# Optimization experiments

Hardware: AMD Instinct MI355X
Metric: run time of the kernel (lower is better)

The kernel has to match this reference:

```python
import jax, jax.numpy as jnp
import numpy as np

B, T, LQ, LC = 8, 256, 20, 10
DIM, H = 128, 8
VDIM, WDIM, CDIM = 1024, 300, 50
WORDS, CHARS = 10000, 100


def _build_edges(T, B):
    """Replicates build_graph_edges(hops=2) + build_semantic_edges + build_query_edges,
    then expand_edge_index_for_batch with num_nodes = T + 1.  Static numpy (jit-safe)."""
    N = T + 1
    es = []
    for h in (1, 2):  # temporal edges, 2 hops (indices replicate original code exactly)
        i = np.arange(T - h)
        es += [np.stack([i, i + h]), np.stack([i + h, i])]
    i = np.arange(T)  # query<->segment edges inside build_graph_edges
    z = np.zeros(T, dtype=np.int64)
    es += [np.stack([z, i + 1]), np.stack([i + 1, z])]
    temporal = np.concatenate(es, axis=1)
    a, b = np.triu_indices(T, k=1)  # torch.combinations(arange(T), r=2)
    sem = np.concatenate([np.stack([a, b]), np.stack([b, a])], axis=1)
    qe = np.stack([np.concatenate([[0], np.arange(1, T + 1)]),
                   np.concatenate([np.arange(1, T + 1), [0]])])
    off = (np.arange(B, dtype=np.int64) * N)[None, :, None]
    expand = lambda e: (e[:, None, :].astype(np.int64) + off).reshape(2, -1)
    return np.concatenate([expand(temporal), expand(sem), expand(qe)], axis=1)


def setup_inputs() -> dict:
    key = jax.random.key(0)
    ks = jax.random.split(key, 16)
    w = lambda k, shape: jax.random.normal(k, shape, jnp.float32) * 0.02
    return {
        "word_ids": jax.random.randint(ks[0], (B, LQ), 0, WORDS),
        "char_ids": jax.random.randint(ks[1], (B, LQ, LC), 0, CHARS),
        "video_features": jax.random.normal(ks[2], (B, T, VDIM), jnp.float32),
        "v_mask": jnp.ones((B, T), jnp.float32),
        "q_mask": jnp.ones((B, LQ), jnp.float32),
        "word_emb": w(ks[3], (WORDS, WDIM)),
        "char_emb": w(ks[4], (CHARS, CDIM)),
        "W_embed": w(ks[5], (WDIM + CDIM, DIM)), "b_embed": jnp.zeros((DIM,), jnp.float32),
        "W_vproj": w(ks[6], (VDIM, DIM)), "b_vproj": jnp.zeros((DIM,), jnp.float32),
        "W_enc": w(ks[7], (DIM, DIM)), "b_enc": jnp.zeros((DIM,), jnp.float32),
        "Wq": w(ks[8], (DIM, DIM)), "bq": jnp.zeros((DIM,), jnp.float32),
        "Wk": w(ks[9], (DIM, DIM)), "bk": jnp.zeros((DIM,), jnp.float32),
        "Wv": w(ks[10], (DIM, DIM)), "bv": jnp.zeros((DIM,), jnp.float32),
        "Wskip": w(ks[11], (DIM, DIM)), "bskip": jnp.zeros((DIM,), jnp.float32),
        "W_start": w(ks[12], (DIM, 1)), "b_start": jnp.zeros((1,), jnp.float32),
        "W_end": w(ks[13], (DIM, 1)), "b_end": jnp.zeros((1,), jnp.float32),
    }


def reference(word_ids, char_ids, video_features, v_mask, q_mask,
              word_emb, char_emb, W_embed, b_embed, W_vproj, b_vproj,
              W_enc, b_enc, Wq, bq, Wk, bk, Wv, bv, Wskip, bskip,
              W_start, b_start, W_end, b_end):
    enc = lambda x, m: jax.nn.relu(x @ W_enc + b_enc) * m[..., None]  # shared feature encoder (stand-in)
    # video branch
    vfeat = enc(video_features @ W_vproj + b_vproj, v_mask)            # [B, T, DIM]
    # query branch: word + char embeddings -> dim, encode, mean-pool
    qemb = jnp.concatenate([word_emb[word_ids], char_emb[char_ids].mean(axis=2)], axis=-1)
    qfeat = enc(qemb @ W_embed + b_embed, q_mask).mean(axis=1)         # [B, DIM]
    nodes = jnp.concatenate([qfeat[:, None, :], vfeat], axis=1)        # [B, N, DIM], N = T+1
    Bn, N, _ = nodes.shape
    Nn = Bn * N
    xf = nodes.reshape(Nn, DIM)
    edges = jnp.asarray(_build_edges(N - 1, Bn))                       # [2, E] static
    src, dst = edges[0], edges[1]                                      # PyG: messages x_j=src -> target i=dst
    hd = DIM // H
    q = (xf @ Wq + bq).reshape(Nn, H, hd)
    k = (xf @ Wk + bk).reshape(Nn, H, hd)
    v = (xf @ Wv + bv).reshape(Nn, H, hd)
    # TransformerConv: per-edge attention logits, segment-softmax over incoming edges
    logits = (q[dst] * k[src]).sum(-1) / float(np.sqrt(hd))            # [E, H]
    mx = jax.ops.segment_max(logits, dst, num_segments=Nn)
    ex = jnp.exp(logits - mx[dst])
    den = jax.ops.segment_sum(ex, dst, num_segments=Nn)
    alpha = ex / (den[dst] + 1e-16)
    agg = jax.ops.segment_sum(alpha[:, :, None] * v[src], dst, num_segments=Nn)  # [Nn, H, hd]
    out = agg.reshape(Nn, DIM) + xf @ Wskip + bskip                    # root_weight skip connection
    out = out.reshape(Bn, N, DIM)
    start_logits = (out[:, 1:] @ W_start + b_start)[..., 0]            # [B, T]
    end_logits = (out[:, 1:] @ W_end + b_end)[..., 0]                  # [B, T]
    return start_logits, end_logits
```

## Files before the change

kernel.cpp:

```cpp
#include <hip/hip_runtime.h>
#include <hip/hip_bf16.h>
#include <math.h>

#define B_ 8
#define T_ 256
#define LQ_ 20
#define LC_ 10
#define DIM_ 128
#define N_ 257
#define NN_ (B_*N_)

#define FMA4(a, s, ww) { (a).x += (s)*(ww).x; (a).y += (s)*(ww).y; (a).z += (s)*(ww).z; (a).w += (s)*(ww).w; }

__global__ __launch_bounds__(512) void kNODE(
    const float* __restrict__ video, const float* __restrict__ Wv,
    const float* __restrict__ bvp,
    const float* __restrict__ We, const float* __restrict__ be,
    const float* __restrict__ vmask,
    const int* __restrict__ word_ids, const int* __restrict__ char_ids,
    const float* __restrict__ word_emb, const float* __restrict__ char_emb,
    const float* __restrict__ W_embed, const float* __restrict__ b_embed,
    const float* __restrict__ q_mask,
    const float* __restrict__ Wq, const float* __restrict__ bq,
    const float* __restrict__ Wk, const float* __restrict__ bk,
    const float* __restrict__ Wvv, const float* __restrict__ bval,
    const float* __restrict__ Ws, const float* __restrict__ bs,
    float* __restrict__ q, float* __restrict__ k,
    float* __restrict__ v, float* __restrict__ sk,
    float* __restrict__ eq)
{
  __shared__ __align__(16) float smem_f[19008];
  float4* ps4 = reinterpret_cast<float4*>(smem_f);
  float* hl = smem_f + 16896;
  float* xe = smem_f + 17952;
  const int blk = blockIdx.x, tid = threadIdx.x;
  const float* Wm[4] = {Wq, Wk, Wvv, Ws};
  const float* bm[4] = {bq, bk, bval, bs};
  float* om[4] = {q, k, v, sk};

  if (blk < 256) {
    const int r0 = blk * 8;
    {
      const float4* src = reinterpret_cast<const float4*>(video + (size_t)r0 * 1024);
      #pragma unroll
      for (int i = 0; i < 4; ++i) {
        const int idx4 = tid + i * 512;
        const int r = idx4 >> 8, f = idx4 & 255;
        *reinterpret_cast<float4*>(&smem_f[r * 1028 + f * 4]) = src[r * 256 + f];
      }
    }
    __syncthreads();
    const int c4 = tid & 31, ks = tid >> 5;
    float4 acc[8];
    #pragma unroll
    for (int r = 0; r < 8; ++r) acc[r] = float4{0.f, 0.f, 0.f, 0.f};
    {
      const float4* W4 = reinterpret_cast<const float4*>(Wv) + c4;
      for (int kc = 0; kc < 16; ++kc) {
        const int k0 = ks * 64 + kc * 4;
        const float4 w0 = W4[(size_t)(k0 + 0) * 32];
        const float4 w1 = W4[(size_t)(k0 + 1) * 32];
        const float4 w2 = W4[(size_t)(k0 + 2) * 32];
        const float4 w3 = W4[(size_t)(k0 + 3) * 32];
        #pragma unroll
        for (int r = 0; r < 8; ++r) {
          const float4 rv = *reinterpret_cast<const float4*>(&smem_f[r * 1028 + k0]);
          FMA4(acc[r], rv.x, w0); FMA4(acc[r], rv.y, w1);
          FMA4(acc[r], rv.z, w2); FMA4(acc[r], rv.w, w3);
        }
      }
    }
    __syncthreads();
    #pragma unroll
    for (int r = 0; r < 8; ++r) ps4[(ks * 8 + r) * 33 + c4] = acc[r];
    __syncthreads();
    if (tid < 256) {
      const int r = tid >> 5, c = tid & 31;
      float4 s = reinterpret_cast<const float4*>(bvp)[c];
      #pragma unroll
      for (int ke = 0; ke < 16; ++ke) {
        const float4 p = ps4[(ke * 8 + r) * 33 + c];
        s.x += p.x; s.y += p.y; s.z += p.z; s.w += p.w;
      }
      *reinterpret_cast<float4*>(&hl[r * 132 + c * 4]) = s;
    }
    __syncthreads();
    #pragma unroll
    for (int r = 0; r < 8; ++r) acc[r] = float4{0.f, 0.f, 0.f, 0.f};
    {
      const float4* We4 = reinterpret_cast<const float4*>(We) + c4;
      #pragma unroll
      for (int kc = 0; kc < 2; ++kc) {
        const int k0 = ks * 8 + kc * 4;
        const float4 w0 = We4[(size_t)(k0 + 0) * 32];
        const float4 w1 = We4[(size_t)(k0 + 1) * 32];
        const float4 w2 = We4[(size_t)(k0 + 2) * 32];
        const float4 w3 = We4[(size_t)(k0 + 3) * 32];
        #pragma unroll
        for (int r = 0; r < 8; ++r) {
          const float4 rv = *reinterpret_cast<const float4*>(&hl[r * 132 + k0]);
          FMA4(acc[r], rv.x, w0); FMA4(acc[r], rv.y, w1);
          FMA4(acc[r], rv.z, w2); FMA4(acc[r], rv.w, w3);
        }
      }
    }
    #pragma unroll
    for (int r = 0; r < 8; ++r) ps4[(ks * 8 + r) * 33 + c4] = acc[r];
    __syncthreads();
    if (tid < 256) {
      const int r = tid >> 5, c = tid & 31;
      float4 s = reinterpret_cast<const float4*>(be)[c];
      #pragma unroll
      for (int ke = 0; ke < 16; ++ke) {
        const float4 p = ps4[(ke * 8 + r) * 33 + c];
        s.x += p.x; s.y += p.y; s.z += p.z; s.w += p.w;
      }
      const float mk = vmask[r0 + r];
      s.x = fmaxf(s.x, 0.f) * mk; s.y = fmaxf(s.y, 0.f) * mk;
      s.z = fmaxf(s.z, 0.f) * mk; s.w = fmaxf(s.w, 0.f) * mk;
      *reinterpret_cast<float4*>(&xe[r * 132 + c * 4]) = s;
    }
    __syncthreads();
    const int m = ks >> 2, keP = ks & 3;
    #pragma unroll
    for (int r = 0; r < 8; ++r) acc[r] = float4{0.f, 0.f, 0.f, 0.f};
    {
      const float4* Wp4 = reinterpret_cast<const float4*>(Wm[m]) + c4;
      #pragma unroll
      for (int kc = 0; kc < 8; ++kc) {
        const int k0 = keP * 32 + kc * 4;
        const float4 w0 = Wp4[(size_t)(k0 + 0) * 32];
        const float4 w1 = Wp4[(size_t)(k0 + 1) * 32];
        const float4 w2 = Wp4[(size_t)(k0 + 2) * 32];
        const float4 w3 = Wp4[(size_t)(k0 + 3) * 32];
        #pragma unroll
        for (int r = 0; r < 8; ++r) {
          const float4 rv = *reinterpret_cast<const float4*>(&xe[r * 132 + k0]);
          FMA4(acc[r], rv.x, w0); FMA4(acc[r], rv.y, w1);
          FMA4(acc[r], rv.z, w2); FMA4(acc[r], rv.w, w3);
        }
      }
    }
    #pragma unroll
    for (int r = 0; r < 8; ++r) ps4[(ks * 8 + r) * 33 + c4] = acc[r];
    __syncthreads();
    #pragma unroll
    for (int it = 0; it < 2; ++it) {
      const int id = tid + it * 512;
      const int mm = id >> 8, r = (id >> 5) & 7, c = id & 31;
      float4 s = reinterpret_cast<const float4*>(bm[mm])[c];
      #pragma unroll
      for (int ke = 0; ke < 4; ++ke) {
        const float4 p = ps4[((mm * 4 + ke) * 8 + r) * 33 + c];
        s.x += p.x; s.y += p.y; s.z += p.z; s.w += p.w;
      }
      const int vr = r0 + r;
      const int node = (vr >> 8) * 257 + 1 + (vr & 255);
      *reinterpret_cast<float4*>(om[mm] + (size_t)node * 128 + 4 * c) = s;
    }
  } else {
    const int qi = blk - 256;
    const int b = qi / 20, lq = qi - b * 20;
    float* emb = smem_f;
    float* ps  = emb + 352;
    float* hq  = emb + 608;
    float* pe  = emb + 736;
    const int wid = word_ids[b * LQ_ + lq];
    for (int m2 = tid; m2 < 300; m2 += 512) emb[m2] = word_emb[(size_t)wid * 300 + m2];
    if (tid < 50) {
      float s = 0.f;
      #pragma unroll
      for (int l = 0; l < 10; ++l) {
        const int cid = char_ids[(b * LQ_ + lq) * 10 + l];
        s += char_emb[cid * 50 + tid];
      }
      emb[300 + tid] = s * 0.1f;
    }
    __syncthreads();
    const int j = tid & 127, half = tid >> 7;
    if (tid < 256) {
      float a = 0.f;
      const float* Wcol = W_embed + (size_t)(half * 175) * 128 + j;
      const float* eh = emb + half * 175;
      #pragma unroll 5
      for (int m2 = 0; m2 < 175; ++m2) a += eh[m2] * Wcol[(size_t)m2 * 128];
      ps[half * 128 + j] = a;
    }
    __syncthreads();
    if (tid < 128) hq[tid] = ps[tid] + ps[128 + tid] + b_embed[tid];
    __syncthreads();
    if (tid < 256) {
      float e = 0.f;
      #pragma unroll 8
      for (int kk = 0; kk < 64; ++kk)
        e += hq[half * 64 + kk] * We[(half * 64 + kk) * 128 + j];
      pe[half * 128 + j] = e;
    }
    __syncthreads();
    if (tid < 128) {
      float ev = pe[tid] + pe[128 + tid] + be[tid];
      ev = fmaxf(ev, 0.f) * q_mask[b * LQ_ + lq];
      eq[(size_t)qi * 128 + tid] = ev;
    }
  }
}

__device__ __forceinline__ float cntf(int dnode, int s) {
  if (dnode == 256) return (s == 0 ? 1.f : 0.f) + (s == 255 ? 1.f : 0.f);
  float c = (s != dnode) ? 1.f : 0.f;
  if (s == 0) c += 1.f;
  if (s == dnode - 1) c += 2.f;
  if (s == dnode + 1 && dnode <= 254) c += 1.f;
  if (s == dnode - 2 && dnode >= 2) c += 1.f;
  if (s == dnode + 2 && dnode <= 253) c += 1.f;
  return c;
}

__global__ __launch_bounds__(256) void kATTN(
    const float* __restrict__ q, const float* __restrict__ k,
    const float* __restrict__ v, const float* __restrict__ eq,
    const float* __restrict__ Wk, const float* __restrict__ bk,
    const float* __restrict__ Wvv, const float* __restrict__ bval,
    const float* __restrict__ W_start, const float* __restrict__ W_end,
    float* __restrict__ nst_p, float* __restrict__ nen_p,
    float* __restrict__ den_p)
{
  __shared__ float Kl[32][128];
  __shared__ float Vl[32][128];
  __shared__ float m0[128];
  __shared__ float vstl[32][8];
  __shared__ float venl[32][8];
  const int d0 = blockIdx.x * 32;
  const int y  = blockIdx.y;
  const int b  = blockIdx.z;
  const int tid = threadIdx.x;
  const int base = b * 257;
  const int s0 = y * 32;
  {
    const float4* ksrc = reinterpret_cast<const float4*>(k + (size_t)(base + s0) * 128);
    const float4* vsrc = reinterpret_cast<const float4*>(v + (size_t)(base + s0) * 128);
    float4* kd = reinterpret_cast<float4*>(Kl);
    float4* vd = reinterpret_cast<float4*>(Vl);
    #pragma unroll
    for (int i = 0; i < 4; ++i) {
      kd[tid + i * 256] = ksrc[tid + i * 256];
      vd[tid + i * 256] = vsrc[tid + i * 256];
    }
  }
  if (y == 0 && tid < 128) {
    float s = 0.f;
    #pragma unroll 4
    for (int lq = 0; lq < LQ_; ++lq) s += eq[((size_t)b * LQ_ + lq) * 128 + tid];
    m0[tid] = s * (1.f / LQ_);
  }
  const int dd = tid >> 3, h = tid & 7;
  const int dnode = d0 + dd + 1;
  const float* qrow = q + (size_t)(base + dnode) * 128 + h * 16;
  const float4 qq0 = *(const float4*)(qrow + 0);
  const float4 qq1 = *(const float4*)(qrow + 4);
  const float4 qq2 = *(const float4*)(qrow + 8);
  const float4 qq3 = *(const float4*)(qrow + 12);
  __syncthreads();
  if (y == 0) {
    const int j = tid & 127, half = tid >> 7;
    const float* W = half ? Wvv : Wk;
    float acc = half ? bval[j] : bk[j];
    #pragma unroll 8
    for (int kk = 0; kk < 128; ++kk) acc += m0[kk] * W[kk * 128 + j];
    if (half) Vl[0][j] = acc; else Kl[0][j] = acc;
  }
  __syncthreads();
  {
    const int sv = tid >> 3, hv = tid & 7;
    const float* vr = &Vl[sv][hv * 16];
    const float* wst = W_start + hv * 16;
    const float* wen = W_end + hv * 16;
    float a = 0.f, e = 0.f;
    #pragma unroll
    for (int i = 0; i < 16; ++i) { a += vr[i] * wst[i]; e += vr[i] * wen[i]; }
    vstl[sv][hv] = a; venl[sv][hv] = e;
  }
  __syncthreads();

  float den = 0.f, nst = 0.f, nen = 0.f;
  #pragma unroll 4
  for (int s = 0; s < 32; ++s) {
    const float* krow = &Kl[s][h * 16];
    const float4 k0 = *(const float4*)(krow + 0);
    const float4 k1 = *(const float4*)(krow + 4);
    const float4 k2 = *(const float4*)(krow + 8);
    const float4 k3 = *(const float4*)(krow + 12);
    float dt = qq0.x*k0.x + qq0.y*k0.y + qq0.z*k0.z + qq0.w*k0.w
             + qq1.x*k1.x + qq1.y*k1.y + qq1.z*k1.z + qq1.w*k1.w
             + qq2.x*k2.x + qq2.y*k2.y + qq2.z*k2.z + qq2.w*k2.w
             + qq3.x*k3.x + qq3.y*k3.y + qq3.z*k3.z + qq3.w*k3.w;
    const float c = cntf(dnode, s0 + s);
    const float pw = c * __expf(dt * 0.25f);
    den += pw;
    nst += pw * vstl[s][h];
    nen += pw * venl[s][h];
  }
  const size_t pb = (((size_t)y * 8 + b) * 256 + d0 + dd) * 8 + h;
  nst_p[pb] = nst; nen_p[pb] = nen; den_p[pb] = den;
}

__global__ __launch_bounds__(256) void kRED(
    const float* __restrict__ nst_p, const float* __restrict__ nen_p,
    const float* __restrict__ den_p, const float* __restrict__ sk,
    const float* __restrict__ W_start, const float* __restrict__ b_start,
    const float* __restrict__ W_end, const float* __restrict__ b_end,
    float* __restrict__ out)
{
  __shared__ float attst[16], atten[16];
  __shared__ float red[16][2][2];
  const int d0 = blockIdx.x * 16;
  const int b = blockIdx.y;
  const int tid = threadIdx.x;
  const int base = b * 257;
  if (tid < 128) {
    const int dd = tid >> 3, h = tid & 7;
    const int dst = d0 + dd;
    float den = 0.f, nst = 0.f, nen = 0.f;
    #pragma unroll
    for (int y = 0; y < 8; ++y) {
      const size_t pb = (((size_t)y * 8 + b) * 256 + dst) * 8 + h;
      nst += nst_p[pb]; nen += nen_p[pb]; den += den_p[pb];
    }
    float rst = nst / (den + 1e-16f);
    float ren = nen / (den + 1e-16f);
    #pragma unroll
    for (int off = 1; off < 8; off <<= 1) {
      rst += __shfl_xor(rst, off);
      ren += __shfl_xor(ren, off);
    }
    if (h == 0) { attst[dd] = rst; atten[dd] = ren; }
  }
  __syncthreads();
  const int jB = tid & 127, shB = tid >> 7;
  const float wst = W_start[jB], wen = W_end[jB];
  #pragma unroll
  for (int dd8 = 0; dd8 < 8; ++dd8) {
    const int dd = shB * 8 + dd8;
    const int dst = d0 + dd;
    const float o = sk[(size_t)(base + dst + 1) * 128 + jB];
    float psum = o * wst, pesum = o * wen;
    #pragma unroll
    for (int off = 1; off < 64; off <<= 1) {
      psum += __shfl_xor(psum, off);
      pesum += __shfl_xor(pesum, off);
    }
    if ((tid & 63) == 0) { red[dd][jB >> 6][0] = psum; red[dd][jB >> 6][1] = pesum; }
  }
  __syncthreads();
  if (tid < 16) {
    out[b * 256 + d0 + tid]        = red[tid][0][0] + red[tid][1][0] + attst[tid] + b_start[0];
    out[2048 + b * 256 + d0 + tid] = red[tid][0][1] + red[tid][1][1] + atten[tid] + b_end[0];
  }
}

extern "C" void kernel_launch(void* const* d_in, const int* in_sizes, int n_in,
                              void* d_out, int out_size, void* d_ws, size_t ws_size,
                              hipStream_t stream) {
  const int*   word_ids = (const int*)d_in[0];
  const int*   char_ids = (const int*)d_in[1];
  const float* video    = (const float*)d_in[2];
  const float* v_mask   = (const float*)d_in[3];
  const float* q_mask   = (const float*)d_in[4];
  const float* word_emb = (const float*)d_in[5];
  const float* char_emb = (const float*)d_in[6];
  const float* W_embed  = (const float*)d_in[7];
  const float* b_embed  = (const float*)d_in[8];
  const float* W_vproj  = (const float*)d_in[9];
  const float* b_vproj  = (const float*)d_in[10];
  const float* W_enc    = (const float*)d_in[11];
  const float* b_enc    = (const float*)d_in[12];
  const float* Wq       = (const float*)d_in[13];
  const float* bq       = (const float*)d_in[14];
  const float* Wk       = (const float*)d_in[15];
  const float* bk       = (const float*)d_in[16];
  const float* Wv       = (const float*)d_in[17];
  const float* bv       = (const float*)d_in[18];
  const float* Wskip    = (const float*)d_in[19];
  const float* bskip    = (const float*)d_in[20];
  const float* W_start  = (const float*)d_in[21];
  const float* b_start  = (const float*)d_in[22];
  const float* W_end    = (const float*)d_in[23];
  const float* b_end    = (const float*)d_in[24];

  float* q     = (float*)d_ws;
  float* k     = q  + NN_ * DIM_;
  float* v     = k  + NN_ * DIM_;
  float* sk    = v  + NN_ * DIM_;
  float* eq    = sk + NN_ * DIM_;
  float* nst_p = eq + 160 * 128;
  float* nen_p = nst_p + 131072;
  float* den_p = nen_p + 131072;

  hipLaunchKernelGGL(kNODE, dim3(416), dim3(512), 0, stream,
    video, W_vproj, b_vproj, W_enc, b_enc, v_mask,
    word_ids, char_ids, word_emb, char_emb, W_embed, b_embed, q_mask,
    Wq, bq, Wk, bk, Wv, bv, Wskip, bskip, q, k, v, sk, eq);
  hipLaunchKernelGGL(kATTN, dim3(8, 8, 8), dim3(256), 0, stream,
    q, k, v, eq, Wk, bk, Wv, bv, W_start, W_end, nst_p, nen_p, den_p);
  hipLaunchKernelGGL(kRED, dim3(16, 8), dim3(256), 0, stream,
    nst_p, nen_p, den_p, sk, W_start, b_start, W_end, b_end, (float*)d_out);
}
```

Before: 58.52 us.

## Fuse attention and reduction kernels into one kernel looping over source chunks

Merges the split-source attention kernel and the partial-sum reduction kernel into a single kernel. Each block now takes 16 destination nodes and loops over all 256 sources in four chunks of 64, reducing partials in shared memory. This removes one launch and the global round trip of the partial buffers. In exchange the grid shrinks from 512 blocks to 128, so parallelism drops. Each block also recomputes the query-node K/V projection, the K/V loads and the per-row value projections that were split across blocks before.

```diff
diff --git a/kernel.cpp b/kernel.cpp
--- a/kernel.cpp
+++ b/kernel.cpp
@@ -216,140 +216,139 @@
   return c;
 }
 
-__global__ __launch_bounds__(256) void kATTN(
+__global__ __launch_bounds__(256) void kATTN3(
     const float* __restrict__ q, const float* __restrict__ k,
     const float* __restrict__ v, const float* __restrict__ eq,
     const float* __restrict__ Wk, const float* __restrict__ bk,
     const float* __restrict__ Wvv, const float* __restrict__ bval,
-    const float* __restrict__ W_start, const float* __restrict__ W_end,
-    float* __restrict__ nst_p, float* __restrict__ nen_p,
-    float* __restrict__ den_p)
+    const float* __restrict__ sk,
+    const float* __restrict__ W_start, const float* __restrict__ b_start,
+    const float* __restrict__ W_end, const float* __restrict__ b_end,
+    float* __restrict__ out)
 {
-  __shared__ float Kl[32][128];
-  __shared__ float Vl[32][128];
+  __shared__ float Kl[64][128];
+  __shared__ float Vl[64][128];
   __shared__ float m0[128];
-  __shared__ float vstl[32][8];
-  __shared__ float venl[32][8];
-  const int d0 = blockIdx.x * 32;
-  const int y  = blockIdx.y;
-  const int b  = blockIdx.z;
+  __shared__ float wstl[128], wenl[128];
+  __shared__ float vstl[64][8], venl[64][8];
+  __shared__ float part[2][16][8][3];
+  __shared__ float attst[16], atten[16];
+  __shared__ float red[16][2][2];
+  const int d0 = blockIdx.x * 16;
+  const int b  = blockIdx.y;
   const int tid = threadIdx.x;
   const int base = b * 257;
-  const int s0 = y * 32;
-  {
-    const float4* ksrc = reinterpret_cast<const float4*>(k + (size_t)(base + s0) * 128);
-    const float4* vsrc = reinterpret_cast<const float4*>(v + (size_t)(base + s0) * 128);
-    float4* kd = reinterpret_cast<float4*>(Kl);
-    float4* vd = reinterpret_cast<float4*>(Vl);
-    #pragma unroll
-    for (int i = 0; i < 4; ++i) {
-      kd[tid + i * 256] = ksrc[tid + i * 256];
-      vd[tid + i * 256] = vsrc[tid + i * 256];
-    }
-  }
-  if (y == 0 && tid < 128) {
+
+  if (tid < 128) {
     float s = 0.f;
     #pragma unroll 4
     for (int lq = 0; lq < LQ_; ++lq) s += eq[((size_t)b * LQ_ + lq) * 128 + tid];
     m0[tid] = s * (1.f / LQ_);
-  }
-  const int dd = tid >> 3, h = tid & 7;
+    wstl[tid] = W_start[tid];
+    wenl[tid] = W_end[tid];
+  }
+  const int sh = tid >> 7, dd = (tid >> 3) & 15, h = tid & 7;
   const int dnode = d0 + dd + 1;
   const float* qrow = q + (size_t)(base + dnode) * 128 + h * 16;
   const float4 qq0 = *(const float4*)(qrow + 0);
   const float4 qq1 = *(const float4*)(qrow + 4);
   const float4 qq2 = *(const float4*)(qrow + 8);
   const float4 qq3 = *(const float4*)(qrow + 12);
+
+  float den = 0.f, nst = 0.f, nen = 0.f;
+  for (int c = 0; c < 4; ++c) {
+    const int s0 = c * 64;
+    __syncthreads();
+    {
+      const float4* ksrc = reinterpret_cast<const float4*>(k + (size_t)(base + s0) * 128);
+      const float4* vsrc = reinterpret_cast<const float4*>(v + (size_t)(base + s0) * 128);
+      float4* kd = reinterpret_cast<float4*>(Kl);
+      float4* vd = reinterpret_cast<float4*>(Vl);
+      #pragma unroll
+      for (int i = 0; i < 8; ++i) {
+        kd[tid + i * 256] = ksrc[tid + i * 256];
+        vd[tid + i * 256] = vsrc[tid + i * 256];
+      }
+    }
+    __syncthreads();
+    if (c == 0) {
+      const int j = tid & 127, half = tid >> 7;
+      const float* W = half ? Wvv : Wk;
+      float acc = half ? bval[j] : bk[j];
+      #pragma unroll 8
+      for (int kk = 0; kk < 128; ++kk) acc += m0[kk] * W[kk * 128 + j];
+      if (half) Vl[0][j] = acc; else Kl[0][j] = acc;
+    }
+    __syncthreads();
+    {
+      const int rv = tid >> 3, hv = tid & 7;
+      #pragma unroll
+      for (int r2 = 0; r2 < 2; ++r2) {
+        const int row = rv + r2 * 32;
+        const float* vr = &Vl[row][hv * 16];
+        const float* ws = &wstl[hv * 16];
+        const float* we = &wenl[hv * 16];
+        float a = 0.f, e = 0.f;
+        #pragma unroll
+        for (int i = 0; i < 16; ++i) { a += vr[i] * ws[i]; e += vr[i] * we[i]; }
+        vstl[row][hv] = a; venl[row][hv] = e;
+      }
+    }
+    __syncthreads();
+    #pragma unroll 4
+    for (int si = 0; si < 32; ++si) {
+      const int sl = sh * 32 + si;
+      const float* krow = &Kl[sl][h * 16];
+      const float4 k0 = *(const float4*)(krow + 0);
+      const float4 k1 = *(const float4*)(krow + 4);
+      const float4 k2 = *(const float4*)(krow + 8);
+      const float4 k3 = *(const float4*)(krow + 12);
+      float dt = qq0.x*k0.x + qq0.y*k0.y + qq0.z*k0.z + qq0.w*k0.w
+               + qq1.x*k1.x + qq1.y*k1.y + qq1.z*k1.z + qq1.w*k1.w
+               + qq2.x*k2.x + qq2.y*k2.y + qq2.z*k2.z + qq2.w*k2.w
+               + qq3.x*k3.x + qq3.y*k3.y + qq3.z*k3.z + qq3.w*k3.w;
+      const float cc = cntf(dnode, s0 + sl);
+      const float pw = cc * __expf(dt * 0.25f);
+      den += pw;
+      nst += pw * vstl[sl][h];
+      nen += pw * venl[sl][h];
+    }
+  }
+  part[sh][dd][h][0] = nst;
+  part[sh][dd][h][1] = nen;
+  part[sh][dd][h][2] = den;
   __syncthreads();
-  if (y == 0) {
-    const int j = tid & 127, half = tid >> 7;
-    const float* W = half ? Wvv : Wk;
-    float acc = half ? bval[j] : bk[j];
-    #pragma unroll 8
-    for (int kk = 0; kk < 128; ++kk) acc += m0[kk] * W[kk * 128 + j];
-    if (half) Vl[0][j] = acc; else Kl[0][j] = acc;
-  }
-  __syncthreads();
-  {
-    const int sv = tid >> 3, hv = tid & 7;
-    const float* vr = &Vl[sv][hv * 16];
-    const float* wst = W_start + hv * 16;
-    const float* wen = W_end + hv * 16;
-    float a = 0.f, e = 0.f;
-    #pragma unroll
-    for (int i = 0; i < 16; ++i) { a += vr[i] * wst[i]; e += vr[i] * wen[i]; }
-    vstl[sv][hv] = a; venl[sv][hv] = e;
-  }
-  __syncthreads();
-
-  float den = 0.f, nst = 0.f, nen = 0.f;
-  #pragma unroll 4
-  for (int s = 0; s < 32; ++s) {
-    const float* krow = &Kl[s][h * 16];
-    const float4 k0 = *(const float4*)(krow + 0);
-    const float4 k1 = *(const float4*)(krow + 4);
-    const float4 k2 = *(const float4*)(krow + 8);
-    const float4 k3 = *(const float4*)(krow + 12);
-    float dt = qq0.x*k0.x + qq0.y*k0.y + qq0.z*k0.z + qq0.w*k0.w
-             + qq1.x*k1.x + qq1.y*k1.y + qq1.z*k1.z + qq1.w*k1.w
-             + qq2.x*k2.x + qq2.y*k2.y + qq2.z*k2.z + qq2.w*k2.w
-             + qq3.x*k3.x + qq3.y*k3.y + qq3.z*k3.z + qq3.w*k3.w;
-    const float c = cntf(dnode, s0 + s);
-    const float pw = c * __expf(dt * 0.25f);
-    den += pw;
-    nst += pw * vstl[s][h];
-    nen += pw * venl[s][h];
-  }
-  const size_t pb = (((size_t)y * 8 + b) * 256 + d0 + dd) * 8 + h;
-  nst_p[pb] = nst; nen_p[pb] = nen; den_p[pb] = den;
-}
-
-__global__ __launch_bounds__(256) void kRED(
-    const float* __restrict__ nst_p, const float* __restrict__ nen_p,
-    const float* __restrict__ den_p, const float* __restrict__ sk,
-    const float* __restrict__ W_start, const float* __restrict__ b_start,
-    const float* __restrict__ W_end, const float* __restrict__ b_end,
-    float* __restrict__ out)
-{
-  __shared__ float attst[16], atten[16];
-  __shared__ float red[16][2][2];
-  const int d0 = blockIdx.x * 16;
-  const int b = blockIdx.y;
-  const int tid = threadIdx.x;
-  const int base = b * 257;
   if (tid < 128) {
-    const int dd = tid >> 3, h = tid & 7;
-    const int dst = d0 + dd;
-    float den = 0.f, nst = 0.f, nen = 0.f;
-    #pragma unroll
-    for (int y = 0; y < 8; ++y) {
-      const size_t pb = (((size_t)y * 8 + b) * 256 + dst) * 8 + h;
-      nst += nst_p[pb]; nen += nen_p[pb]; den += den_p[pb];
-    }
-    float rst = nst / (den + 1e-16f);
-    float ren = nen / (den + 1e-16f);
+    const int dd2 = tid >> 3, h2 = tid & 7;
+    const float n1 = part[0][dd2][h2][0] + part[1][dd2][h2][0];
+    const float n2 = part[0][dd2][h2][1] + part[1][dd2][h2][1];
+    const float dn = part[0][dd2][h2][2] + part[1][dd2][h2][2];
+    float rst = n1 / (dn + 1e-16f);
+    float ren = n2 / (dn + 1e-16f);
     #pragma unroll
     for (int off = 1; off < 8; off <<= 1) {
       rst += __shfl_xor(rst, off);
       ren += __shfl_xor(ren, off);
     }
-    if (h == 0) { attst[dd] = rst; atten[dd] = ren; }
+    if (h2 == 0) { attst[dd2] = rst; atten[dd2] = ren; }
   }
   __syncthreads();
-  const int jB = tid & 127, shB = tid >> 7;
-  const float wst = W_start[jB], wen = W_end[jB];
-  #pragma unroll
-  for (int dd8 = 0; dd8 < 8; ++dd8) {
-    const int dd = shB * 8 + dd8;
-    const int dst = d0 + dd;
-    const float o = sk[(size_t)(base + dst + 1) * 128 + jB];
-    float psum = o * wst, pesum = o * wen;
-    #pragma unroll
-    for (int off = 1; off < 64; off <<= 1) {
-      psum += __shfl_xor(psum, off);
-      pesum += __shfl_xor(pesum, off);
-    }
-    if ((tid & 63) == 0) { red[dd][jB >> 6][0] = psum; red[dd][jB >> 6][1] = pesum; }
+  {
+    const int jB = tid & 127, shB = tid >> 7;
+    const float wst = wstl[jB], wen = wenl[jB];
+    #pragma unroll
+    for (int dd8 = 0; dd8 < 8; ++dd8) {
+      const int ddx = shB * 8 + dd8;
+      const int dst = d0 + ddx;
+      const float o = sk[(size_t)(base + dst + 1) * 128 + jB];
+      float psum = o * wst, pesum = o * wen;
+      #pragma unroll
+      for (int off = 1; off < 64; off <<= 1) {
+        psum += __shfl_xor(psum, off);
+        pesum += __shfl_xor(pesum, off);
+      }
+      if ((tid & 63) == 0) { red[ddx][jB >> 6][0] = psum; red[ddx][jB >> 6][1] = pesum; }
+    }
   }
   __syncthreads();
   if (tid < 16) {
@@ -392,16 +391,12 @@
   float* v     = k  + NN_ * DIM_;
   float* sk    = v  + NN_ * DIM_;
   float* eq    = sk + NN_ * DIM_;
-  float* nst_p = eq + 160 * 128;
-  float* nen_p = nst_p + 131072;
-  float* den_p = nen_p + 131072;
 
   hipLaunchKernelGGL(kNODE, dim3(416), dim3(512), 0, stream,
     video, W_vproj, b_vproj, W_enc, b_enc, v_mask,
     word_ids, char_ids, word_emb, char_emb, W_embed, b_embed, q_mask,
     Wq, bq, Wk, bk, Wv, bv, Wskip, bskip, q, k, v, sk, eq);
-  hipLaunchKernelGGL(kATTN, dim3(8, 8, 8), dim3(256), 0, stream,
-    q, k, v, eq, Wk, bk, Wv, bv, W_start, W_end, nst_p, nen_p, den_p);
-  hipLaunchKernelGGL(kRED, dim3(16, 8), dim3(256), 0, stream,
-    nst_p, nen_p, den_p, sk, W_start, b_start, W_end, b_end, (float*)d_out);
+  hipLaunchKernelGGL(kATTN3, dim3(16, 8), dim3(256), 0, stream,
+    q, k, v, eq, Wk, bk, Wv, bv, sk, W_start, b_start, W_end, b_end,
+    (float*)d_out);
 }
```

Measured after the change: 72.00 us. +23.0%, slower.
